# Optimization experiments

Measured on AMD Instinct MI355X. Metric: run time of the kernel, lower is better.

## Reference

```python
import jax, jax.numpy as jnp
import numpy as np

TEMPERATURE = 0.1
NSAMPLE = 32
B, N_PER, M_PER, C_FEAT = 2, 16384, 4096, 64


def setup_inputs() -> dict:
    key = jax.random.key(0)
    ks = jax.random.split(key, 4)
    xyz = jax.random.normal(ks[0], (B * N_PER, 3), jnp.float32)
    new_xyz = jax.random.normal(ks[1], (B * M_PER, 3), jnp.float32)
    new_xyz_r = jax.random.uniform(ks[2], (B * M_PER, 1), jnp.float32, minval=0.5, maxval=1.0)
    features = jax.random.normal(ks[3], (B * N_PER, C_FEAT), jnp.float32)
    xyz_batch_cnt = jnp.full((B,), N_PER, jnp.int32)
    new_xyz_batch_cnt = jnp.full((B,), M_PER, jnp.int32)
    temperature_decay = jnp.ones((1,), jnp.float32)
    return dict(xyz=xyz, xyz_batch_cnt=xyz_batch_cnt, new_xyz=new_xyz,
                new_xyz_r=new_xyz_r, new_xyz_batch_cnt=new_xyz_batch_cnt,
                features=features, temperature_decay=temperature_decay)


def _ball_query(xyz_b, new_xyz_b, r_b, nsample):
    # xyz_b: (B,N,3), new_xyz_b: (B,M,3), r_b: (B,M)
    # Returns idx (B,M,nsample) int32 (batch-local point indices, first-in-order
    # within the ball, remaining slots filled with first hit, 0 if empty) and
    # empty mask (B,M) bool. Mirrors the CUDA ball_query_deform kernel.
    N = xyz_b.shape[1]
    d2 = jnp.sum((new_xyz_b[:, :, None, :] - xyz_b[:, None, :, :]) ** 2, axis=-1)  # (B,M,N)
    within = d2 < (r_b ** 2)[..., None]
    # key = point index if within radius else N; top_k of -key gives the first
    # nsample in-ball indices in ascending index order.
    key = jnp.where(within, jnp.arange(N, dtype=jnp.int32), jnp.int32(N))
    neg_vals, _ = jax.lax.top_k(-key, nsample)
    cand = -neg_vals  # (B,M,nsample)
    cnt = within.sum(axis=-1)  # (B,M)
    slot_valid = jnp.arange(nsample) < cnt[..., None]
    idx = jnp.where(slot_valid, cand, cand[..., :1])  # pad with first found index
    empty = cnt == 0
    idx = jnp.where(empty[..., None], 0, idx)
    return idx.astype(jnp.int32), empty


def reference(xyz, xyz_batch_cnt, new_xyz, new_xyz_r, new_xyz_batch_cnt, features, temperature_decay):
    b = xyz_batch_cnt.shape[0]
    n = xyz.shape[0] // b
    m = new_xyz.shape[0] // b
    c = features.shape[1]
    real_t = TEMPERATURE * temperature_decay[0]
    explore_r = new_xyz_r + real_t * 5.0  # (M_tot, 1)

    xyz_b = xyz.reshape(b, n, 3)
    nxyz_b = new_xyz.reshape(b, m, 3)
    idx_b, empty_b = _ball_query(xyz_b, nxyz_b, explore_r.reshape(b, m), NSAMPLE)

    gather = jax.vmap(lambda pts, i: pts[i])  # per-batch gather

    grouped_xyz = gather(xyz_b, idx_b)                 # (B,M,ns,3)
    grouped_xyz = grouped_xyz - nxyz_b[:, :, None, :]  # center
    grouped_xyz = jnp.where(empty_b[:, :, None, None], 0.0, grouped_xyz)
    grouped_xyz = grouped_xyz.reshape(b * m, NSAMPLE, 3).transpose(0, 2, 1)  # (M_tot,3,ns)

    dist_xyz = jnp.sqrt(jnp.sum(grouped_xyz * grouped_xyz, axis=1))  # (M_tot,ns)
    weights = 1.0 - jax.nn.sigmoid((dist_xyz - new_xyz_r) / real_t)  # (M_tot,ns)

    feat_b = features.reshape(b, n, c)
    grouped_feat = gather(feat_b, idx_b)  # (B,M,ns,C)
    grouped_feat = jnp.where(empty_b[:, :, None, None], 0.0, grouped_feat)
    grouped_feat = grouped_feat.reshape(b * m, NSAMPLE, c).transpose(0, 2, 1)  # (M_tot,C,ns)

    new_features = jnp.concatenate([grouped_xyz, grouped_feat], axis=1)  # (M_tot,3+C,ns)
    idx = idx_b.reshape(b * m, NSAMPLE)
    return new_features, weights, idx
```

## Files before the change

### kernel.cpp

```cpp
#include <hip/hip_runtime.h>
#include <math.h>

#define NS 32
#define WPB 4
#define SCAN0 2048
#define TSTRIDE 36

__device__ __forceinline__ void write_query(
    int m, int bb, bool empty, int lane,
    const int* sIdxW, float* sT,
    const float* __restrict__ xyz, const float* __restrict__ new_xyz,
    const float* __restrict__ new_xyz_r, const float* __restrict__ features,
    float real_t, float* __restrict__ out, int N_per, int C, int M_tot)
{
#pragma clang fp contract(off)
    const float* xb = xyz + (size_t)bb * N_per * 3;
    const int    j  = lane & 31;
    const size_t nf_base = (size_t)m * (3 + C) * NS;
    float* wout = out + (size_t)M_tot * (3 + C) * NS;
    float* iout = wout + (size_t)M_tot * NS;

    if (lane < NS) {
        const float qx = new_xyz[(size_t)m * 3 + 0];
        const float qy = new_xyz[(size_t)m * 3 + 1];
        const float qz = new_xyz[(size_t)m * 3 + 2];
        const float r_orig = new_xyz_r[m];
        const int pj = empty ? 0 : sIdxW[j];
        float gx = 0.f, gy = 0.f, gz = 0.f;
        if (!empty) {
            gx = xb[(size_t)pj * 3 + 0] - qx;
            gy = xb[(size_t)pj * 3 + 1] - qy;
            gz = xb[(size_t)pj * 3 + 2] - qz;
        }
        float d2 = gx * gx;
        d2 = d2 + gy * gy;
        d2 = d2 + gz * gz;
        float dist = sqrtf(d2);
        float wt = 1.0f / (1.0f + expf((dist - r_orig) / real_t));
        out[nf_base + 0 * NS + j] = gx;
        out[nf_base + 1 * NS + j] = gy;
        out[nf_base + 2 * NS + j] = gz;
        wout[(size_t)m * NS + j] = wt;
        iout[(size_t)m * NS + j] = (float)pj;
    }

    const float* fb = features + (size_t)bb * N_per * C;
    int c0 = 0;
    for (; c0 + 32 <= C; c0 += 32) {
        const int k  = lane & 7;
        const int f4 = 4 * (k & 3);
        #pragma unroll
        for (int t = 0; t < 4; ++t) {
            const int r  = 8 * t + (lane >> 3);
            const int pj = empty ? 0 : sIdxW[r];
            float4 v = make_float4(0.f, 0.f, 0.f, 0.f);
            if (!empty) v = *(const float4*)(fb + (size_t)pj * C + c0 + 4 * k);
            const int rs = r ^ f4;
            sT[(4 * k + 0) * TSTRIDE + rs] = v.x;
            sT[(4 * k + 1) * TSTRIDE + rs] = v.y;
            sT[(4 * k + 2) * TSTRIDE + rs] = v.z;
            sT[(4 * k + 3) * TSTRIDE + rs] = v.w;
        }
        const int jg = lane & 7;
        #pragma unroll
        for (int s2 = 0; s2 < 4; ++s2) {
            const int ch = 8 * s2 + (lane >> 3);
            const int jb = (4 * jg) ^ (4 * ((ch >> 2) & 3));
            float4 w = *(const float4*)&sT[ch * TSTRIDE + jb];
            *(float4*)&out[nf_base + (size_t)(3 + c0 + ch) * NS + 4 * jg] = w;
        }
    }
    if (c0 < C) {
        const int h  = lane >> 5;
        const int pj = empty ? 0 : sIdxW[j];
        const float* frow = fb + (size_t)pj * C;
        for (int c = c0 + h; c < C; c += 2) {
            float v = empty ? 0.f : frow[c];
            out[nf_base + (size_t)(3 + c) * NS + j] = v;
        }
    }
}

__global__ __launch_bounds__(256) void qgd_AC(
    const float* __restrict__ xyz, const float* __restrict__ new_xyz,
    const float* __restrict__ new_xyz_r, const float* __restrict__ features,
    const float* __restrict__ tdec, float* __restrict__ out,
    int* __restrict__ counter, int* __restrict__ list,
    int N_per, int M_per, int C, int M_tot)
{
#pragma clang fp contract(off)
    __shared__ __align__(16) float sBuf[WPB * 32 * TSTRIDE];
    __shared__ int sIdx[WPB][NS];

    const int lane = threadIdx.x & 63;
    const int wv   = threadIdx.x >> 6;
    const int m    = blockIdx.x * WPB + wv;
    if (m >= M_tot) return;

    const int bb = m / M_per;
    const float* xb = xyz + (size_t)bb * N_per * 3;
    const float qx = new_xyz[(size_t)m * 3 + 0];
    const float qy = new_xyz[(size_t)m * 3 + 1];
    const float qz = new_xyz[(size_t)m * 3 + 2];
    const float real_t = 0.1f * tdec[0];
    const float er  = new_xyz_r[m] + real_t * 5.0f;
    const float er2 = er * er;
    const unsigned long long lt = (1ull << lane) - 1ull;

    const int scan0 = (SCAN0 < N_per) ? SCAN0 : N_per;
    int cnt = 0;
    for (int base = 0; base < scan0; base += 256) {
        float d2k[4];
        #pragma unroll
        for (int k = 0; k < 4; ++k) {
            int p = base + k * 64 + lane;
            int pc = (p < N_per) ? p : (N_per - 1);
            const float* pp = xb + (size_t)pc * 3;
            float dx = pp[0] - qx, dy = pp[1] - qy, dz = pp[2] - qz;
            float d2 = dx * dx;
            d2 = d2 + dy * dy;
            d2 = d2 + dz * dz;
            d2k[k] = (p < N_per) ? d2 : 1e30f;
        }
        #pragma unroll
        for (int k = 0; k < 4; ++k) {
            bool hit = d2k[k] < er2;
            unsigned long long msk = __ballot(hit);
            if (hit) {
                int slot = cnt + (int)__popcll(msk & lt);
                if (slot < NS) sIdx[wv][slot] = base + k * 64 + lane;
            }
            cnt += (int)__popcll(msk);
        }
        if (cnt >= NS) break;
    }

    if (cnt >= NS) {
        write_query(m, bb, false, lane, sIdx[wv],
                    sBuf + wv * (32 * TSTRIDE),
                    xyz, new_xyz, new_xyz_r, features, real_t, out,
                    N_per, C, M_tot);
    } else if (lane == 0) {
        int pos = atomicAdd(counter, 1);
        list[pos] = m;
    }
}

__global__ __launch_bounds__(256) void qgd_B(
    const float* __restrict__ xyz, const float* __restrict__ new_xyz,
    const float* __restrict__ new_xyz_r, const float* __restrict__ features,
    const float* __restrict__ tdec, float* __restrict__ out,
    const int* __restrict__ counter, const int* __restrict__ list,
    int N_per, int M_per, int C, int M_tot)
{
#pragma clang fp contract(off)
    __shared__ int sH[WPB][NS];
    __shared__ int sC[WPB];
    __shared__ int sM[NS];
    __shared__ int sTot;
    __shared__ __align__(16) float sT[32 * TSTRIDE];

    const int lane = threadIdx.x & 63;
    const int wv   = threadIdx.x >> 6;
    const int nstrag = *counter;
    const unsigned long long lt = (1ull << lane) - 1ull;
    const float real_t = 0.1f * tdec[0];

    for (int it = blockIdx.x; it < nstrag; it += gridDim.x) {
        const int m  = list[it];
        const int bb = m / M_per;
        const float* xb = xyz + (size_t)bb * N_per * 3;
        const float qx = new_xyz[(size_t)m * 3 + 0];
        const float qy = new_xyz[(size_t)m * 3 + 1];
        const float qz = new_xyz[(size_t)m * 3 + 2];
        const float er  = new_xyz_r[m] + real_t * 5.0f;
        const float er2 = er * er;

        const int rb = (int)(((long long)N_per * wv) / WPB);
        const int re = (int)(((long long)N_per * (wv + 1)) / WPB);

        int cnt = 0;
        for (int base = rb; base < re; base += 256) {
            float d2k[4];
            #pragma unroll
            for (int k = 0; k < 4; ++k) {
                int p = base + k * 64 + lane;
                int pc = (p < re) ? p : (re - 1);
                const float* pp = xb + (size_t)pc * 3;
                float dx = pp[0] - qx, dy = pp[1] - qy, dz = pp[2] - qz;
                float d2 = dx * dx;
                d2 = d2 + dy * dy;
                d2 = d2 + dz * dz;
                d2k[k] = (p < re) ? d2 : 1e30f;
            }
            #pragma unroll
            for (int k = 0; k < 4; ++k) {
                bool hit = d2k[k] < er2;
                unsigned long long msk = __ballot(hit);
                if (hit) {
                    int slot = cnt + (int)__popcll(msk & lt);
                    if (slot < NS) sH[wv][slot] = base + k * 64 + lane;
                }
                cnt += (int)__popcll(msk);
            }
            if (cnt >= NS) break;
        }
        if (lane == 0) sC[wv] = (cnt < NS) ? cnt : NS;
        __syncthreads();

        if (threadIdx.x < NS) {
            const int j  = threadIdx.x;
            const int c0 = sC[0], c1 = sC[1], c2 = sC[2], c3 = sC[3];
            const int o1 = c0, o2 = c0 + c1, o3 = o2 + c2;
            const int tot = o3 + c3;
            int v = 0;
            if (j < tot) {
                if      (j >= o3) v = sH[3][j - o3];
                else if (j >= o2) v = sH[2][j - o2];
                else if (j >= o1) v = sH[1][j - o1];
                else              v = sH[0][j];
            }
            int first = 0;
            if      (c0 > 0) first = sH[0][0];
            else if (c1 > 0) first = sH[1][0];
            else if (c2 > 0) first = sH[2][0];
            else if (c3 > 0) first = sH[3][0];
            sM[j] = (tot == 0) ? 0 : ((j < tot) ? v : first);
            if (j == 0) sTot = tot;
        }
        __syncthreads();

        if (wv == 0) {
            write_query(m, bb, (sTot == 0), lane, sM, sT,
                        xyz, new_xyz, new_xyz_r, features, real_t, out,
                        N_per, C, M_tot);
        }
        __syncthreads();
    }
}

extern "C" void kernel_launch(void* const* d_in, const int* in_sizes, int n_in,
                              void* d_out, int out_size, void* d_ws, size_t ws_size,
                              hipStream_t stream) {
    const float* xyz       = (const float*)d_in[0];
    const float* new_xyz   = (const float*)d_in[2];
    const float* new_xyz_r = (const float*)d_in[3];
    const float* features  = (const float*)d_in[5];
    const float* tdec      = (const float*)d_in[6];

    const int B     = in_sizes[1];
    const int N_tot = in_sizes[0] / 3;
    const int M_tot = in_sizes[2] / 3;
    const int C     = in_sizes[5] / N_tot;
    const int N_per = N_tot / B;
    const int M_per = M_tot / B;

    float* out     = (float*)d_out;
    int*   counter = (int*)d_ws;
    int*   list    = (int*)d_ws + 4;

    hipMemsetAsync(counter, 0, sizeof(int), stream);

    const int blocksA = (M_tot + WPB - 1) / WPB;
    qgd_AC<<<blocksA, 256, 0, stream>>>(xyz, new_xyz, new_xyz_r, features,
                                        tdec, out, counter, list,
                                        N_per, M_per, C, M_tot);
    qgd_B<<<512, 256, 0, stream>>>(xyz, new_xyz, new_xyz_r, features,
                                   tdec, out, counter, list,
                                   N_per, M_per, C, M_tot);
}
```

Baseline: 119.2 us.

## Fuse fast-path and straggler ball-query kernels into one block-local kernel

Merges the two-kernel scheme into a single kernel. Before, a first pass wrote straggler queries to a global list via atomics and a second kernel rescanned them. Now each block finishes its own stragglers right away: all four waves split the full point range for each straggling query in the block. This removes the memset, the atomic list and the second launch with its serialization. The trade-off is that straggler work is no longer load-balanced across blocks, so blocks that hold stragglers run longer while others idle.

New measurement: 121.9 us. 2.3% more time.

```diff
diff --git a/kernel.cpp b/kernel.cpp
--- a/kernel.cpp
+++ b/kernel.cpp
@@ -81,93 +81,30 @@
     }
 }
 
-__global__ __launch_bounds__(256) void qgd_AC(
+__global__ __launch_bounds__(256) void qgd_fused(
     const float* __restrict__ xyz, const float* __restrict__ new_xyz,
     const float* __restrict__ new_xyz_r, const float* __restrict__ features,
     const float* __restrict__ tdec, float* __restrict__ out,
-    int* __restrict__ counter, int* __restrict__ list,
     int N_per, int M_per, int C, int M_tot)
 {
 #pragma clang fp contract(off)
     __shared__ __align__(16) float sBuf[WPB * 32 * TSTRIDE];
     __shared__ int sIdx[WPB][NS];
+    __shared__ int sH[WPB][NS];
+    __shared__ int sC[WPB];
+    __shared__ int sStrag[WPB];
+    __shared__ int sM[NS];
+    __shared__ int sTot;
 
     const int lane = threadIdx.x & 63;
     const int wv   = threadIdx.x >> 6;
     const int m    = blockIdx.x * WPB + wv;
-    if (m >= M_tot) return;
-
-    const int bb = m / M_per;
-    const float* xb = xyz + (size_t)bb * N_per * 3;
-    const float qx = new_xyz[(size_t)m * 3 + 0];
-    const float qy = new_xyz[(size_t)m * 3 + 1];
-    const float qz = new_xyz[(size_t)m * 3 + 2];
-    const float real_t = 0.1f * tdec[0];
-    const float er  = new_xyz_r[m] + real_t * 5.0f;
-    const float er2 = er * er;
-    const unsigned long long lt = (1ull << lane) - 1ull;
-
-    const int scan0 = (SCAN0 < N_per) ? SCAN0 : N_per;
-    int cnt = 0;
-    for (int base = 0; base < scan0; base += 256) {
-        float d2k[4];
-        #pragma unroll
-        for (int k = 0; k < 4; ++k) {
-            int p = base + k * 64 + lane;
-            int pc = (p < N_per) ? p : (N_per - 1);
-            const float* pp = xb + (size_t)pc * 3;
-            float dx = pp[0] - qx, dy = pp[1] - qy, dz = pp[2] - qz;
-            float d2 = dx * dx;
-            d2 = d2 + dy * dy;
-            d2 = d2 + dz * dz;
-            d2k[k] = (p < N_per) ? d2 : 1e30f;
-        }
-        #pragma unroll
-        for (int k = 0; k < 4; ++k) {
-            bool hit = d2k[k] < er2;
-            unsigned long long msk = __ballot(hit);
-            if (hit) {
-                int slot = cnt + (int)__popcll(msk & lt);
-                if (slot < NS) sIdx[wv][slot] = base + k * 64 + lane;
-            }
-            cnt += (int)__popcll(msk);
-        }
-        if (cnt >= NS) break;
-    }
-
-    if (cnt >= NS) {
-        write_query(m, bb, false, lane, sIdx[wv],
-                    sBuf + wv * (32 * TSTRIDE),
-                    xyz, new_xyz, new_xyz_r, features, real_t, out,
-                    N_per, C, M_tot);
-    } else if (lane == 0) {
-        int pos = atomicAdd(counter, 1);
-        list[pos] = m;
-    }
-}
-
-__global__ __launch_bounds__(256) void qgd_B(
-    const float* __restrict__ xyz, const float* __restrict__ new_xyz,
-    const float* __restrict__ new_xyz_r, const float* __restrict__ features,
-    const float* __restrict__ tdec, float* __restrict__ out,
-    const int* __restrict__ counter, const int* __restrict__ list,
-    int N_per, int M_per, int C, int M_tot)
-{
-#pragma clang fp contract(off)
-    __shared__ int sH[WPB][NS];
-    __shared__ int sC[WPB];
-    __shared__ int sM[NS];
-    __shared__ int sTot;
-    __shared__ __align__(16) float sT[32 * TSTRIDE];
-
-    const int lane = threadIdx.x & 63;
-    const int wv   = threadIdx.x >> 6;
-    const int nstrag = *counter;
+    const bool active = (m < M_tot);
     const unsigned long long lt = (1ull << lane) - 1ull;
     const float real_t = 0.1f * tdec[0];
 
-    for (int it = blockIdx.x; it < nstrag; it += gridDim.x) {
-        const int m  = list[it];
+    int cnt = 0;
+    if (active) {
         const int bb = m / M_per;
         const float* xb = xyz + (size_t)bb * N_per * 3;
         const float qx = new_xyz[(size_t)m * 3 + 0];
@@ -176,10 +113,58 @@
         const float er  = new_xyz_r[m] + real_t * 5.0f;
         const float er2 = er * er;
 
+        const int scan0 = (SCAN0 < N_per) ? SCAN0 : N_per;
+        for (int base = 0; base < scan0; base += 256) {
+            float d2k[4];
+            #pragma unroll
+            for (int k = 0; k < 4; ++k) {
+                int p = base + k * 64 + lane;
+                int pc = (p < N_per) ? p : (N_per - 1);
+                const float* pp = xb + (size_t)pc * 3;
+                float dx = pp[0] - qx, dy = pp[1] - qy, dz = pp[2] - qz;
+                float d2 = dx * dx;
+                d2 = d2 + dy * dy;
+                d2 = d2 + dz * dz;
+                d2k[k] = (p < N_per) ? d2 : 1e30f;
+            }
+            #pragma unroll
+            for (int k = 0; k < 4; ++k) {
+                bool hit = d2k[k] < er2;
+                unsigned long long msk = __ballot(hit);
+                if (hit) {
+                    int slot = cnt + (int)__popcll(msk & lt);
+                    if (slot < NS) sIdx[wv][slot] = base + k * 64 + lane;
+                }
+                cnt += (int)__popcll(msk);
+            }
+            if (cnt >= NS) break;
+        }
+
+        if (cnt >= NS) {
+            write_query(m, bb, false, lane, sIdx[wv],
+                        sBuf + wv * (32 * TSTRIDE),
+                        xyz, new_xyz, new_xyz_r, features, real_t, out,
+                        N_per, C, M_tot);
+        }
+    }
+    if (lane == 0) sStrag[wv] = (active && cnt < NS) ? 1 : 0;
+    __syncthreads();
+
+    for (int s = 0; s < WPB; ++s) {
+        if (!sStrag[s]) continue;
+        const int ms = blockIdx.x * WPB + s;
+        const int bb = ms / M_per;
+        const float* xb = xyz + (size_t)bb * N_per * 3;
+        const float qx = new_xyz[(size_t)ms * 3 + 0];
+        const float qy = new_xyz[(size_t)ms * 3 + 1];
+        const float qz = new_xyz[(size_t)ms * 3 + 2];
+        const float er  = new_xyz_r[ms] + real_t * 5.0f;
+        const float er2 = er * er;
+
         const int rb = (int)(((long long)N_per * wv) / WPB);
         const int re = (int)(((long long)N_per * (wv + 1)) / WPB);
 
-        int cnt = 0;
+        int c2 = 0;
         for (int base = rb; base < re; base += 256) {
             float d2k[4];
             #pragma unroll
@@ -198,21 +183,21 @@
                 bool hit = d2k[k] < er2;
                 unsigned long long msk = __ballot(hit);
                 if (hit) {
-                    int slot = cnt + (int)__popcll(msk & lt);
+                    int slot = c2 + (int)__popcll(msk & lt);
                     if (slot < NS) sH[wv][slot] = base + k * 64 + lane;
                 }
-                cnt += (int)__popcll(msk);
-            }
-            if (cnt >= NS) break;
-        }
-        if (lane == 0) sC[wv] = (cnt < NS) ? cnt : NS;
+                c2 += (int)__popcll(msk);
+            }
+            if (c2 >= NS) break;
+        }
+        if (lane == 0) sC[wv] = (c2 < NS) ? c2 : NS;
         __syncthreads();
 
         if (threadIdx.x < NS) {
             const int j  = threadIdx.x;
-            const int c0 = sC[0], c1 = sC[1], c2 = sC[2], c3 = sC[3];
-            const int o1 = c0, o2 = c0 + c1, o3 = o2 + c2;
-            const int tot = o3 + c3;
+            const int q0 = sC[0], q1 = sC[1], q2 = sC[2], q3 = sC[3];
+            const int o1 = q0, o2 = q0 + q1, o3 = o2 + q2;
+            const int tot = o3 + q3;
             int v = 0;
             if (j < tot) {
                 if      (j >= o3) v = sH[3][j - o3];
@@ -221,17 +206,17 @@
                 else              v = sH[0][j];
             }
             int first = 0;
-            if      (c0 > 0) first = sH[0][0];
-            else if (c1 > 0) first = sH[1][0];
-            else if (c2 > 0) first = sH[2][0];
-            else if (c3 > 0) first = sH[3][0];
+            if      (q0 > 0) first = sH[0][0];
+            else if (q1 > 0) first = sH[1][0];
+            else if (q2 > 0) first = sH[2][0];
+            else if (q3 > 0) first = sH[3][0];
             sM[j] = (tot == 0) ? 0 : ((j < tot) ? v : first);
             if (j == 0) sTot = tot;
         }
         __syncthreads();
 
         if (wv == 0) {
-            write_query(m, bb, (sTot == 0), lane, sM, sT,
+            write_query(ms, bb, (sTot == 0), lane, sM, sBuf,
                         xyz, new_xyz, new_xyz_r, features, real_t, out,
                         N_per, C, M_tot);
         }
@@ -255,17 +240,8 @@
     const int N_per = N_tot / B;
     const int M_per = M_tot / B;
 
-    float* out     = (float*)d_out;
-    int*   counter = (int*)d_ws;
-    int*   list    = (int*)d_ws + 4;
-
-    hipMemsetAsync(counter, 0, sizeof(int), stream);
-
-    const int blocksA = (M_tot + WPB - 1) / WPB;
-    qgd_AC<<<blocksA, 256, 0, stream>>>(xyz, new_xyz, new_xyz_r, features,
-                                        tdec, out, counter, list,
-                                        N_per, M_per, C, M_tot);
-    qgd_B<<<512, 256, 0, stream>>>(xyz, new_xyz, new_xyz_r, features,
-                                   tdec, out, counter, list,
-                                   N_per, M_per, C, M_tot);
+    const int blocks = (M_tot + WPB - 1) / WPB;
+    qgd_fused<<<blocks, 256, 0, stream>>>(xyz, new_xyz, new_xyz_r, features,
+                                          tdec, (float*)d_out,
+                                          N_per, M_per, C, M_tot);
 }
```
